# Optimization experiments

Hardware: AMD Instinct MI355X
Metric: run time of the kernel (lower is better)

## Reference

```python
import jax, jax.numpy as jnp
import numpy as np

NUM_HEADS = 16
D_MODEL = 1024
HEAD_DIM = D_MODEL // NUM_HEADS
B, S = 2, 2048


def setup_inputs() -> dict:
    key = jax.random.key(0)
    ks = jax.random.split(key, 11)
    scale = 1.0 / np.sqrt(D_MODEL)
    inp = {
        'query': jax.random.normal(ks[0], (B, S, D_MODEL), jnp.float32),
        'key': jax.random.normal(ks[1], (B, S, D_MODEL), jnp.float32),
        'value': jax.random.normal(ks[2], (B, S, D_MODEL), jnp.float32),
        'Wq': jax.random.normal(ks[3], (D_MODEL, D_MODEL), jnp.float32) * scale,
        'bq': jnp.zeros((D_MODEL,), jnp.float32),
        'Wk': jax.random.normal(ks[4], (D_MODEL, D_MODEL), jnp.float32) * scale,
        'bk': jnp.zeros((D_MODEL,), jnp.float32),
        'Wv': jax.random.normal(ks[5], (D_MODEL, D_MODEL), jnp.float32) * scale,
        'bv': jnp.zeros((D_MODEL,), jnp.float32),
        'Wo': jax.random.normal(ks[6], (D_MODEL, D_MODEL), jnp.float32) * scale,
        'bo': jnp.zeros((D_MODEL,), jnp.float32),
    }
    return inp


def reference(query, key, value, Wq, bq, Wk, bk, Wv, bv, Wo, bo):
    b, s, _ = query.shape
    # Linear projections (torch Linear: x @ W.T + b; here W stored as [in,out])
    Q = query @ Wq + bq
    K = key @ Wk + bk
    V = value @ Wv + bv
    # [B, H, S, Dh]
    Q = Q.reshape(b, s, NUM_HEADS, HEAD_DIM).transpose(0, 2, 1, 3)
    K = K.reshape(b, -1, NUM_HEADS, HEAD_DIM).transpose(0, 2, 1, 3)
    V = V.reshape(b, -1, NUM_HEADS, HEAD_DIM).transpose(0, 2, 1, 3)
    scores = jnp.einsum('bhqd,bhkd->bhqk', Q, K) / jnp.sqrt(jnp.float32(HEAD_DIM)).astype(Q.dtype)
    attn = jax.nn.softmax(scores, axis=-1)
    ctx = jnp.einsum('bhqk,bhkd->bhqd', attn, V)
    ctx = ctx.transpose(0, 2, 1, 3).reshape(b, s, D_MODEL)
    return ctx @ Wo + bo
```

## Files before the change

### kernel.cpp

```cpp
#include <hip/hip_runtime.h>
#include <hip/hip_bf16.h>
#include <math.h>

#define NUM_HEADS 16
#define D_MODEL 1024
#define HEAD_DIM 64
#define BATCH 2
#define SEQ 2048
#define M_TOTAL (BATCH*SEQ)

typedef __bf16 bf16;
typedef __bf16 bf16x2 __attribute__((ext_vector_type(2)));
typedef __bf16 bf16x4 __attribute__((ext_vector_type(4)));
typedef __bf16 bf16x8 __attribute__((ext_vector_type(8)));
typedef float  floatx4  __attribute__((ext_vector_type(4)));
typedef float  floatx16 __attribute__((ext_vector_type(16)));

#define CLSCALE 0.180336884f

__device__ __forceinline__ void async_copy16(const bf16* g, bf16* l) {
    __builtin_amdgcn_global_load_lds(
        (const __attribute__((address_space(1))) void*)g,
        (__attribute__((address_space(3))) void*)l, 16, 0, 0);
}

__global__ __launch_bounds__(256)
void convert_kernel(const float* __restrict__ Wq, const float* __restrict__ Wk,
                    const float* __restrict__ Wv, const float* __restrict__ Wo,
                    const float* __restrict__ q, const float* __restrict__ k,
                    const float* __restrict__ v,
                    bf16* __restrict__ Wt, bf16* __restrict__ Xb)
{
    const int blk = blockIdx.x;
    const int tid = threadIdx.x;
    if (blk < 256) {
        const int wi  = blk >> 6;
        const int sub = blk & 63;
        const int xb  = sub & 3;
        const int yb  = sub >> 2;
        const float* W = (wi == 0) ? Wq : (wi == 1) ? Wk : (wi == 2) ? Wv : Wo;
        bf16* dstM = Wt + (size_t)wi * D_MODEL * D_MODEL;
        const int n  = xb * 256 + tid;
        const int k0 = yb * 64;
        bf16* dst = dstM + (size_t)n * D_MODEL + k0;
        #pragma unroll
        for (int jc = 0; jc < 8; ++jc) {
            bf16x8 w;
            #pragma unroll
            for (int j = 0; j < 8; ++j)
                w[j] = (bf16)W[(size_t)(k0 + jc * 8 + j) * D_MODEL + n];
            *(bf16x8*)(dst + jc * 8) = w;
        }
    } else {
        const int rem   = blk - 256;
        const int plane = rem >> 11;
        const int xb    = rem & 2047;
        const float* X = (plane == 0) ? q : (plane == 1) ? k : v;
        bf16* dst = Xb + (size_t)plane * M_TOTAL * D_MODEL;
        size_t i = ((size_t)xb * 256 + tid) * 8;
        const float4 u = *(const float4*)(X + i);
        const float4 w = *(const float4*)(X + i + 4);
        bf16x8 o;
        o[0] = (bf16)u.x; o[1] = (bf16)u.y; o[2] = (bf16)u.z; o[3] = (bf16)u.w;
        o[4] = (bf16)w.x; o[5] = (bf16)w.y; o[6] = (bf16)w.z; o[7] = (bf16)w.w;
        *(bf16x8*)(dst + i) = o;
    }
}

__global__ __launch_bounds__(256)
void proj_kernel(const bf16* __restrict__ Xb, const bf16* __restrict__ Wt,
                 const float* __restrict__ bq, const float* __restrict__ bk,
                 const float* __restrict__ bv,
                 bf16* __restrict__ Qo, bf16* __restrict__ Ko, bf16* __restrict__ Vto)
{
    const int lin  = blockIdx.x;
    const int xcd  = lin & 7;
    const int idx  = lin >> 3;
    const int nt   = idx & 7;
    const int t2   = idx >> 3;
    const int mloc = t2 & 3;
    const int which= t2 >> 2;
    const int tileM = (xcd * 4 + mloc) * 128;
    const int tileN = nt * 128;

    const bf16* X     = Xb + (size_t)which * M_TOTAL * D_MODEL;
    const bf16* Wm    = Wt + (size_t)which * D_MODEL * D_MODEL;
    const float* bias = (which == 0) ? bq : (which == 1) ? bk : bv;

    const int tid  = threadIdx.x;
    const int lane = tid & 63;
    const int wave = tid >> 6;
    const int quad = lane >> 4;
    const int l16  = lane & 15;

    __shared__ bf16 sA[128 * 32];
    __shared__ bf16 sB[128 * 32];

    floatx4 acc[4][4];
    const floatx4 z4 = {0.0f, 0.0f, 0.0f, 0.0f};
    #pragma unroll
    for (int i = 0; i < 4; i++)
        #pragma unroll
        for (int j = 0; j < 4; j++) acc[i][j] = z4;

    const int wm = (wave >> 1) * 64;
    const int wn = (wave & 1) * 64;

    const int c0   = wave * 64 + lane;
    const int row0 = c0 >> 2, col0 = (c0 & 3) * 8;
    const int c1   = c0 + 256;
    const int row1 = c1 >> 2, col1 = (c1 & 3) * 8;
    bf16* ldsA0 = sA + (size_t)(wave * 64) * 8;
    bf16* ldsA1 = sA + (size_t)(256 + wave * 64) * 8;
    bf16* ldsB0 = sB + (size_t)(wave * 64) * 8;
    bf16* ldsB1 = sB + (size_t)(256 + wave * 64) * 8;

    for (int k0 = 0; k0 < D_MODEL; k0 += 32) {
        __syncthreads();
        async_copy16(X  + (size_t)(tileM + row0) * D_MODEL + k0 + col0, ldsA0);
        async_copy16(X  + (size_t)(tileM + row1) * D_MODEL + k0 + col1, ldsA1);
        async_copy16(Wm + (size_t)(tileN + row0) * D_MODEL + k0 + col0, ldsB0);
        async_copy16(Wm + (size_t)(tileN + row1) * D_MODEL + k0 + col1, ldsB1);
        __syncthreads();

        bf16x8 af[4], bfr[4];
        #pragma unroll
        for (int i = 0; i < 4; i++) af[i]  = *(const bf16x8*)&sA[(wm + i * 16 + l16) * 32 + quad * 8];
        #pragma unroll
        for (int j = 0; j < 4; j++) bfr[j] = *(const bf16x8*)&sB[(wn + j * 16 + l16) * 32 + quad * 8];
        if (which != 2) {
            #pragma unroll
            for (int i = 0; i < 4; i++)
                #pragma unroll
                for (int j = 0; j < 4; j++)
                    acc[i][j] = __builtin_amdgcn_mfma_f32_16x16x32_bf16(af[i], bfr[j], acc[i][j], 0, 0, 0);
        } else {
            #pragma unroll
            for (int i = 0; i < 4; i++)
                #pragma unroll
                for (int j = 0; j < 4; j++)
                    acc[i][j] = __builtin_amdgcn_mfma_f32_16x16x32_bf16(bfr[i], af[j], acc[i][j], 0, 0, 0);
        }
    }

    if (which != 2) {
        bf16* out = (which == 0) ? Qo : Ko;
        const float oscale = (which == 0) ? CLSCALE : 1.0f;
        #pragma unroll
        for (int i = 0; i < 4; i++) {
            int mbase = tileM + wm + i * 16 + quad * 4;
            #pragma unroll
            for (int j = 0; j < 4; j++) {
                int n = tileN + wn + j * 16 + l16;
                float bb = bias[n];
                int h = n >> 6, d = n & 63;
                #pragma unroll
                for (int r = 0; r < 4; r++) {
                    int mm = mbase + r;
                    int b = mm >> 11, s = mm & 2047;
                    out[(((size_t)(b * NUM_HEADS + h)) * SEQ + s) * HEAD_DIM + d] =
                        (bf16)((acc[i][j][r] + bb) * oscale);
                }
            }
        }
    } else {
        #pragma unroll
        for (int i = 0; i < 4; i++) {
            #pragma unroll
            for (int r = 0; r < 4; r++) {
                int n = tileN + wn + i * 16 + quad * 4 + r;
                float bb = bias[n];
                int h = n >> 6, d = n & 63;
                #pragma unroll
                for (int j = 0; j < 4; j++) {
                    int m = tileM + wm + j * 16 + l16;
                    int b = m >> 11, s = m & 2047;
                    Vto[(((size_t)(b * NUM_HEADS + h)) * HEAD_DIM + d) * SEQ + s] =
                        (bf16)(acc[i][j][r] + bb);
                }
            }
        }
    }
}

__global__ __launch_bounds__(256)
void attn_kernel(const bf16* __restrict__ Q, const bf16* __restrict__ K,
                 const bf16* __restrict__ Vt, bf16* __restrict__ Ctx)
{
    const int lin    = blockIdx.x;
    const int xcd    = lin & 7;
    const int rest   = lin >> 3;
    const int superg = rest >> 5;
    const int qi     = rest & 31;
    const int bh     = superg * 8 + xcd;
    const int b      = bh >> 4, h = bh & 15;
    const int q0     = qi * 64;

    const int tid  = threadIdx.x;
    const int lane = tid & 63;
    const int wave = tid >> 6;
    const int half = lane >> 5;
    const int m31  = lane & 31;
    const int xs   = m31 & 7;

    const int qsub  = wave & 1;
    const int kjsub = wave >> 1;

    __shared__ bf16 sQP[64][72];
    __shared__ bf16 sK[64 * 64];
    __shared__ bf16 sVt[64 * 64];
    __shared__ float sL[64];

    const bf16* Qb  = Q  + ((size_t)bh * SEQ + q0) * HEAD_DIM;
    const bf16* Kb  = K  + (size_t)bh * SEQ * HEAD_DIM;
    const bf16* Vtb = Vt + (size_t)bh * HEAD_DIM * SEQ;

    #pragma unroll
    for (int it = 0; it < 2; ++it) {
        int g   = tid + it * 256;
        int row = g >> 3;
        int c   = (g & 7) * 8;
        *(bf16x8*)&sQP[row][c] = *(const bf16x8*)(Qb + (size_t)row * HEAD_DIM + c);
    }
    __syncthreads();

    bf16x8 bQ[4];
    #pragma unroll
    for (int s = 0; s < 4; s++)
        bQ[s] = *(const bf16x8*)&sQP[qsub * 32 + m31][s * 16 + half * 8];

    floatx16 o0, o1;
    #pragma unroll
    for (int r = 0; r < 16; r++) { o0[r] = 0.0f; o1[r] = 0.0f; }
    float lp = 0.0f;

    for (int kt = 0; kt < SEQ / 64; ++kt) {
        __syncthreads();
        #pragma unroll
        for (int it = 0; it < 2; ++it) {
            int c    = tid + it * 256;
            int row  = c >> 3;
            int scol = ((c & 7) ^ (row & 7)) * 8;
            async_copy16(Kb  + (size_t)(kt * 64 + row) * HEAD_DIM + scol,
                         sK + (size_t)c * 8);
            async_copy16(Vtb + (size_t)row * SEQ + kt * 64 + scol,
                         sVt + (size_t)c * 8);
        }
        __syncthreads();

        floatx16 sc;
        #pragma unroll
        for (int r = 0; r < 16; r++) sc[r] = 0.0f;
        #pragma unroll
        for (int s = 0; s < 4; s++) {
            bf16x8 a = *(const bf16x8*)&sK[(kjsub * 32 + m31) * 64 + (((2 * s + half) ^ xs) * 8)];
            sc = __builtin_amdgcn_mfma_f32_32x32x16_bf16(a, bQ[s], sc, 0, 0, 0);
        }

        #pragma unroll
        for (int r = 0; r < 16; r++) sc[r] = exp2f(sc[r]);
        float ls = 0.0f;
        #pragma unroll
        for (int r = 0; r < 16; r++) ls += sc[r];
        lp += ls;

        #pragma unroll
        for (int rg = 0; rg < 4; rg++) {
            bf16x4 pk;
            #pragma unroll
            for (int i = 0; i < 4; i++) pk[i] = (bf16)sc[rg * 4 + i];
            *(bf16x4*)&sQP[qsub * 32 + m31][kjsub * 32 + rg * 8 + half * 4] = pk;
        }

        bf16x8 bP[2];
        #pragma unroll
        for (int s = 0; s < 2; s++)
            bP[s] = *(const bf16x8*)&sQP[qsub * 32 + m31][kjsub * 32 + s * 16 + half * 8];

        #pragma unroll
        for (int s = 0; s < 2; s++) {
            int ch = ((4 * kjsub + 2 * s + half) ^ xs) * 8;
            bf16x8 a0 = *(const bf16x8*)&sVt[(size_t)m31 * 64 + ch];
            bf16x8 a1 = *(const bf16x8*)&sVt[(size_t)(32 + m31) * 64 + ch];
            o0 = __builtin_amdgcn_mfma_f32_32x32x16_bf16(a0, bP[s], o0, 0, 0, 0);
            o1 = __builtin_amdgcn_mfma_f32_32x32x16_bf16(a1, bP[s], o1, 0, 0, 0);
        }
    }

    lp += __shfl_xor(lp, 32, 64);

    __syncthreads();
    float* fO = (qsub == 0) ? (float*)sK : (float*)sVt;
    if (kjsub == 1) {
        #pragma unroll
        for (int r = 0; r < 16; r++) {
            fO[r * 64 + lane]        = o0[r];
            fO[1024 + r * 64 + lane] = o1[r];
        }
        if (half == 0) sL[qsub * 32 + m31] = lp;
    }
    __syncthreads();
    if (kjsub == 0) {
        #pragma unroll
        for (int r = 0; r < 16; r++) {
            o0[r] += fO[r * 64 + lane];
            o1[r] += fO[1024 + r * 64 + lane];
        }
        float denom = lp + sL[qsub * 32 + m31];
        float inv = 1.0f / denom;

        int q = q0 + qsub * 32 + m31;
        size_t base = ((size_t)b * SEQ + q) * D_MODEL + h * HEAD_DIM;
        #pragma unroll
        for (int rg = 0; rg < 4; rg++) {
            int d0 = rg * 8 + half * 4;
            bf16x4 w0, w1;
            #pragma unroll
            for (int i = 0; i < 4; i++) {
                w0[i] = (bf16)(o0[rg * 4 + i] * inv);
                w1[i] = (bf16)(o1[rg * 4 + i] * inv);
            }
            *(bf16x4*)&Ctx[base + d0]      = w0;
            *(bf16x4*)&Ctx[base + 32 + d0] = w1;
        }
    }
}

__global__ __launch_bounds__(256)
void out_proj_kernel(const bf16* __restrict__ A, const bf16* __restrict__ Wto,
                     const float* __restrict__ bias, float* __restrict__ Out)
{
    const int lin  = blockIdx.x;
    const int xcd  = lin & 7;
    const int idx  = lin >> 3;
    const int nt   = idx & 7;
    const int mloc = idx >> 3;
    const int tileM = (xcd * 8 + mloc) * 64;
    const int tileN = nt * 128;

    const int tid  = threadIdx.x;
    const int lane = tid & 63;
    const int wave = tid >> 6;
    const int quad = lane >> 4;
    const int l16  = lane & 15;

    __shared__ bf16 sA[64 * 32];
    __shared__ bf16 sB[128 * 32];

    floatx4 acc[2][4];
    const floatx4 z4 = {0.0f, 0.0f, 0.0f, 0.0f};
    #pragma unroll
    for (int i = 0; i < 2; i++)
        #pragma unroll
        for (int j = 0; j < 4; j++) acc[i][j] = z4;

    const int wm = (wave >> 1) * 32;
    const int wn = (wave & 1) * 64;

    const int c0   = wave * 64 + lane;
    const int row0 = c0 >> 2, col0 = (c0 & 3) * 8;
    const int c1   = c0 + 256;
    const int row1 = c1 >> 2, col1 = (c1 & 3) * 8;
    bf16* ldsA0 = sA + (size_t)(wave * 64) * 8;
    bf16* ldsB0 = sB + (size_t)(wave * 64) * 8;
    bf16* ldsB1 = sB + (size_t)(256 + wave * 64) * 8;

    for (int k0 = 0; k0 < D_MODEL; k0 += 32) {
        __syncthreads();
        async_copy16(A   + (size_t)(tileM + row0) * D_MODEL + k0 + col0, ldsA0);
        async_copy16(Wto + (size_t)(tileN + row0) * D_MODEL + k0 + col0, ldsB0);
        async_copy16(Wto + (size_t)(tileN + row1) * D_MODEL + k0 + col1, ldsB1);
        __syncthreads();

        bf16x8 af[2], bfr[4];
        #pragma unroll
        for (int i = 0; i < 2; i++) af[i]  = *(const bf16x8*)&sA[(wm + i * 16 + l16) * 32 + quad * 8];
        #pragma unroll
        for (int j = 0; j < 4; j++) bfr[j] = *(const bf16x8*)&sB[(wn + j * 16 + l16) * 32 + quad * 8];
        #pragma unroll
        for (int i = 0; i < 2; i++)
            #pragma unroll
            for (int j = 0; j < 4; j++)
                acc[i][j] = __builtin_amdgcn_mfma_f32_16x16x32_bf16(af[i], bfr[j], acc[i][j], 0, 0, 0);
    }

    #pragma unroll
    for (int i = 0; i < 2; i++) {
        int mbase = tileM + wm + i * 16 + quad * 4;
        #pragma unroll
        for (int j = 0; j < 4; j++) {
            int n = tileN + wn + j * 16 + l16;
            float bb = bias[n];
            #pragma unroll
            for (int r = 0; r < 4; r++)
                Out[(size_t)(mbase + r) * D_MODEL + n] = acc[i][j][r] + bb;
        }
    }
}

extern "C" void kernel_launch(void* const* d_in, const int* in_sizes, int n_in,
                              void* d_out, int out_size, void* d_ws, size_t ws_size,
                              hipStream_t stream)
{
    const float* q  = (const float*)d_in[0];
    const float* k  = (const float*)d_in[1];
    const float* v  = (const float*)d_in[2];
    const float* Wq = (const float*)d_in[3];
    const float* bq = (const float*)d_in[4];
    const float* Wk = (const float*)d_in[5];
    const float* bk = (const float*)d_in[6];
    const float* Wv = (const float*)d_in[7];
    const float* bv = (const float*)d_in[8];
    const float* Wo = (const float*)d_in[9];
    const float* bo = (const float*)d_in[10];
    float* out = (float*)d_out;

    const size_t PLANE = (size_t)M_TOTAL * D_MODEL;
    bf16* Qb = (bf16*)d_ws;
    bf16* Kb = Qb + PLANE;
    bf16* Vt = Kb + PLANE;
    bf16* Cb = Vt + PLANE;
    bf16* Wt = Cb + PLANE;
    bf16* Xb = Wt + 4 * (size_t)D_MODEL * D_MODEL;

    convert_kernel<<<dim3(6400), 256, 0, stream>>>(Wq, Wk, Wv, Wo, q, k, v, Wt, Xb);
    proj_kernel<<<dim3(768), 256, 0, stream>>>(Xb, Wt, bq, bk, bv, Qb, Kb, Vt);
    attn_kernel<<<dim3(1024), 256, 0, stream>>>(Qb, Kb, Vt, Cb);
    out_proj_kernel<<<dim3(512), 256, 0, stream>>>(Cb, Wt + 3 * (size_t)D_MODEL * D_MODEL, bo, out);
}
```

Measured before the change: 247.7 us.

## Double-buffer K/V tiles and transpose P in registers via permlane32 swap

The attention kernel now keeps two LDS buffers each for K and V. It issues the async global-to-LDS copies for the next tile before computing on the current one, so the second barrier per iteration goes away. The P tile is packed to bf16 and rearranged across lanes with permlane32_swap instead of a write and re-read through shared memory. Q fragments are loaded straight from global memory. The change also adds s_setprio around the MFMA sections and uses the hardware exp2 builtin. In exchange, LDS use doubles, and correctness depends on the permlane layout matching the MFMA B-operand layout.

```diff
diff --git a/kernel.cpp b/kernel.cpp
--- a/kernel.cpp
+++ b/kernel.cpp
@@ -15,13 +15,26 @@
 typedef __bf16 bf16x8 __attribute__((ext_vector_type(8)));
 typedef float  floatx4  __attribute__((ext_vector_type(4)));
 typedef float  floatx16 __attribute__((ext_vector_type(16)));
+typedef unsigned int uintx2 __attribute__((ext_vector_type(2)));
+typedef unsigned int uintx4 __attribute__((ext_vector_type(4)));
 
 #define CLSCALE 0.180336884f
+
+#if __has_builtin(__builtin_amdgcn_exp2f)
+#define EXP2(x) __builtin_amdgcn_exp2f(x)
+#else
+#define EXP2(x) exp2f(x)
+#endif
 
 __device__ __forceinline__ void async_copy16(const bf16* g, bf16* l) {
     __builtin_amdgcn_global_load_lds(
         (const __attribute__((address_space(1))) void*)g,
         (__attribute__((address_space(3))) void*)l, 16, 0, 0);
+}
+
+__device__ __forceinline__ unsigned pk2(float lo, float hi) {
+    bf16x2 t; t[0] = (bf16)lo; t[1] = (bf16)hi;
+    return __builtin_bit_cast(unsigned, t);
 }
 
 __global__ __launch_bounds__(256)
@@ -206,28 +219,27 @@
     const int qsub  = wave & 1;
     const int kjsub = wave >> 1;
 
-    __shared__ bf16 sQP[64][72];
-    __shared__ bf16 sK[64 * 64];
-    __shared__ bf16 sVt[64 * 64];
+    __shared__ bf16 sK[2][64 * 64];
+    __shared__ bf16 sV[2][64 * 64];
     __shared__ float sL[64];
 
     const bf16* Qb  = Q  + ((size_t)bh * SEQ + q0) * HEAD_DIM;
     const bf16* Kb  = K  + (size_t)bh * SEQ * HEAD_DIM;
     const bf16* Vtb = Vt + (size_t)bh * HEAD_DIM * SEQ;
 
+    bf16x8 bQ[4];
+    #pragma unroll
+    for (int s = 0; s < 4; s++)
+        bQ[s] = *(const bf16x8*)(Qb + (size_t)(qsub * 32 + m31) * HEAD_DIM + s * 16 + half * 8);
+
     #pragma unroll
     for (int it = 0; it < 2; ++it) {
-        int g   = tid + it * 256;
-        int row = g >> 3;
-        int c   = (g & 7) * 8;
-        *(bf16x8*)&sQP[row][c] = *(const bf16x8*)(Qb + (size_t)row * HEAD_DIM + c);
-    }
-    __syncthreads();
-
-    bf16x8 bQ[4];
-    #pragma unroll
-    for (int s = 0; s < 4; s++)
-        bQ[s] = *(const bf16x8*)&sQP[qsub * 32 + m31][s * 16 + half * 8];
+        int c    = tid + it * 256;
+        int row  = c >> 3;
+        int scol = ((c & 7) ^ (row & 7)) * 8;
+        async_copy16(Kb  + (size_t)row * HEAD_DIM + scol, &sK[0][c * 8]);
+        async_copy16(Vtb + (size_t)row * SEQ + scol,      &sV[0][c * 8]);
+    }
 
     floatx16 o0, o1;
     #pragma unroll
@@ -235,62 +247,74 @@
     float lp = 0.0f;
 
     for (int kt = 0; kt < SEQ / 64; ++kt) {
+        const int p = kt & 1;
         __syncthreads();
-        #pragma unroll
-        for (int it = 0; it < 2; ++it) {
-            int c    = tid + it * 256;
-            int row  = c >> 3;
-            int scol = ((c & 7) ^ (row & 7)) * 8;
-            async_copy16(Kb  + (size_t)(kt * 64 + row) * HEAD_DIM + scol,
-                         sK + (size_t)c * 8);
-            async_copy16(Vtb + (size_t)row * SEQ + kt * 64 + scol,
-                         sVt + (size_t)c * 8);
-        }
-        __syncthreads();
+
+        bf16x8 aK[4];
+        #pragma unroll
+        for (int s = 0; s < 4; s++)
+            aK[s] = *(const bf16x8*)&sK[p][(kjsub * 32 + m31) * 64 + (((2 * s + half) ^ xs) * 8)];
+
+        if (kt + 1 < SEQ / 64) {
+            #pragma unroll
+            for (int it = 0; it < 2; ++it) {
+                int c    = tid + it * 256;
+                int row  = c >> 3;
+                int scol = ((c & 7) ^ (row & 7)) * 8;
+                async_copy16(Kb  + (size_t)((kt + 1) * 64 + row) * HEAD_DIM + scol,
+                             &sK[p ^ 1][c * 8]);
+                async_copy16(Vtb + (size_t)row * SEQ + (kt + 1) * 64 + scol,
+                             &sV[p ^ 1][c * 8]);
+            }
+        }
 
         floatx16 sc;
         #pragma unroll
         for (int r = 0; r < 16; r++) sc[r] = 0.0f;
-        #pragma unroll
-        for (int s = 0; s < 4; s++) {
-            bf16x8 a = *(const bf16x8*)&sK[(kjsub * 32 + m31) * 64 + (((2 * s + half) ^ xs) * 8)];
-            sc = __builtin_amdgcn_mfma_f32_32x32x16_bf16(a, bQ[s], sc, 0, 0, 0);
-        }
-
-        #pragma unroll
-        for (int r = 0; r < 16; r++) sc[r] = exp2f(sc[r]);
+        __builtin_amdgcn_s_setprio(1);
+        #pragma unroll
+        for (int s = 0; s < 4; s++)
+            sc = __builtin_amdgcn_mfma_f32_32x32x16_bf16(aK[s], bQ[s], sc, 0, 0, 0);
+        __builtin_amdgcn_s_setprio(0);
+
+        #pragma unroll
+        for (int r = 0; r < 16; r++) sc[r] = EXP2(sc[r]);
         float ls = 0.0f;
         #pragma unroll
         for (int r = 0; r < 16; r++) ls += sc[r];
         lp += ls;
 
-        #pragma unroll
-        for (int rg = 0; rg < 4; rg++) {
-            bf16x4 pk;
-            #pragma unroll
-            for (int i = 0; i < 4; i++) pk[i] = (bf16)sc[rg * 4 + i];
-            *(bf16x4*)&sQP[qsub * 32 + m31][kjsub * 32 + rg * 8 + half * 4] = pk;
-        }
-
         bf16x8 bP[2];
         #pragma unroll
-        for (int s = 0; s < 2; s++)
-            bP[s] = *(const bf16x8*)&sQP[qsub * 32 + m31][kjsub * 32 + s * 16 + half * 8];
-
+        for (int s = 0; s < 2; s++) {
+            const int bs = 8 * s;
+            unsigned x = pk2(sc[bs + 0], sc[bs + 1]);
+            unsigned z = pk2(sc[bs + 2], sc[bs + 3]);
+            unsigned y = pk2(sc[bs + 4], sc[bs + 5]);
+            unsigned w = pk2(sc[bs + 6], sc[bs + 7]);
+            auto r0 = __builtin_amdgcn_permlane32_swap(x, y, false, false);
+            auto r1 = __builtin_amdgcn_permlane32_swap(z, w, false, false);
+            uintx4 bp;
+            bp[0] = r0[0]; bp[1] = r1[0]; bp[2] = r0[1]; bp[3] = r1[1];
+            bP[s] = __builtin_bit_cast(bf16x8, bp);
+        }
+
+        __builtin_amdgcn_s_setprio(1);
         #pragma unroll
         for (int s = 0; s < 2; s++) {
             int ch = ((4 * kjsub + 2 * s + half) ^ xs) * 8;
-            bf16x8 a0 = *(const bf16x8*)&sVt[(size_t)m31 * 64 + ch];
-            bf16x8 a1 = *(const bf16x8*)&sVt[(size_t)(32 + m31) * 64 + ch];
+            bf16x8 a0 = *(const bf16x8*)&sV[p][(size_t)m31 * 64 + ch];
+            bf16x8 a1 = *(const bf16x8*)&sV[p][(size_t)(32 + m31) * 64 + ch];
             o0 = __builtin_amdgcn_mfma_f32_32x32x16_bf16(a0, bP[s], o0, 0, 0, 0);
             o1 = __builtin_amdgcn_mfma_f32_32x32x16_bf16(a1, bP[s], o1, 0, 0, 0);
         }
+        __builtin_amdgcn_s_setprio(0);
     }
 
     lp += __shfl_xor(lp, 32, 64);
 
     __syncthreads();
-    float* fO = (qsub == 0) ? (float*)sK : (float*)sVt;
+    float* fO = (qsub == 0) ? (float*)&sK[0][0] : (float*)&sK[1][0];
     if (kjsub == 1) {
         #pragma unroll
         for (int r = 0; r < 16; r++) {
```

Result: faster. 236.9 us (-4.4%).
